# Performance work log

Measured on AMD Instinct MI355X. Metric: run time of the kernel, lower is better.

## Reference

```python
import jax, jax.numpy as jnp
from jax import lax
import numpy as np

EPS = 1e-5  # BatchNorm eps


def setup_inputs() -> dict:
    key = jax.random.key(0)
    ks = jax.random.split(key, 8)
    N, C_in, T, V = 64, 64, 300, 25
    C_out, K, KT = 64, 3, 9
    x = jax.random.normal(ks[0], (N, C_in, T, V), dtype=jnp.float32)
    A = jax.random.uniform(ks[1], (K, V, V), dtype=jnp.float32)
    # 1x1 conv weight squeezed to [K*C_out, C_in]
    w_gcn = jax.random.normal(ks[2], (K * C_out, C_in), dtype=jnp.float32) * (1.0 / np.sqrt(C_in))
    b_gcn = jax.random.normal(ks[3], (K * C_out,), dtype=jnp.float32) * 0.01
    # temporal conv weight [O, I, kT, 1]
    w_tcn = jax.random.normal(ks[4], (C_out, C_out, KT, 1), dtype=jnp.float32) * (1.0 / np.sqrt(C_out * KT))
    b_tcn = jax.random.normal(ks[5], (C_out,), dtype=jnp.float32) * 0.01
    gamma = jnp.ones((C_out,), dtype=jnp.float32)
    beta = jnp.zeros((C_out,), dtype=jnp.float32)
    return {"x": x, "A": A, "w_gcn": w_gcn, "b_gcn": b_gcn,
            "w_tcn": w_tcn, "b_tcn": b_tcn, "gamma": gamma, "beta": beta}


def reference(x, A, w_gcn, b_gcn, w_tcn, b_tcn, gamma, beta):
    K = A.shape[0]
    # unit_gcn: 1x1 conv (pointwise over channels) then spatial graph aggregation
    y = jnp.einsum('nctv,oc->notv', x, w_gcn) + b_gcn[None, :, None, None]  # [N, K*C, T, V]
    n, kc, t, v = y.shape
    y = y.reshape(n, K, kc // K, t, v)
    y = jnp.einsum('nkctv,kvw->nctw', y, A)  # [N, C, T, V]
    # unit_tcn: temporal conv (kernel 9x1, pad 4) + BatchNorm (training mode: batch stats)
    pad = (w_tcn.shape[2] - 1) // 2
    y = lax.conv_general_dilated(y, w_tcn, window_strides=(1, 1),
                                 padding=((pad, pad), (0, 0)),
                                 dimension_numbers=('NCHW', 'OIHW', 'NCHW'))
    y = y + b_tcn[None, :, None, None]
    mean = jnp.mean(y, axis=(0, 2, 3), keepdims=True)
    var = jnp.var(y, axis=(0, 2, 3), keepdims=True)
    y = (y - mean) * lax.rsqrt(var + EPS) * gamma[None, :, None, None] + beta[None, :, None, None]
    # residual (identity: in==out, stride==1) + ReLU
    return jax.nn.relu(y + x)
```

## Files before the change

### kernel.cpp

```cpp
#include <hip/hip_runtime.h>
#include <hip/hip_bf16.h>

#define N_    64
#define C_    64
#define T_    300
#define V_    25
#define K_    3
#define KT_   9
#define PAD_  4

typedef short bf16x8 __attribute__((ext_vector_type(8)));
typedef float f32x4  __attribute__((ext_vector_type(4)));

static __device__ __forceinline__ unsigned short f2bf(float f) {
    __hip_bfloat16 h = __float2bfloat16(f);
    return __builtin_bit_cast(unsigned short, h);
}
static __device__ __forceinline__ unsigned int pk2(float a, float b) {
    return (unsigned int)f2bf(a) | ((unsigned int)f2bf(b) << 16);
}
static __device__ __forceinline__ float bfhi(unsigned int u) {
    return __builtin_bit_cast(float, u << 16);
}
static __device__ __forceinline__ float bflo(unsigned int u) {
    return __builtin_bit_cast(float, u & 0xffff0000u);
}
static __device__ __forceinline__ float bf2f(unsigned short u) {
    return __builtin_bit_cast(float, (unsigned int)u << 16);
}

__global__ __launch_bounds__(256) void prep_kernel(
    const float* __restrict__ Wt, const float* __restrict__ Wg,
    const float* __restrict__ bg, const float* __restrict__ A,
    unsigned short* __restrict__ Wtb, unsigned short* __restrict__ Wgbt,
    unsigned short* __restrict__ bias2b, unsigned short* __restrict__ Abt)
{
    int i = blockIdx.x * 256 + threadIdx.x;
    if (i < 9*64*64) {
        int kt = i >> 12, r = i & 4095, o = r >> 6, c = r & 63;
        Wtb[i] = f2bf(Wt[(size_t)(o*64 + c)*9 + kt]);
    }
    int j = i - 9*64*64;
    if (j >= 0 && j < 64*192) {
        int o = j / 192, kc = j - 192*(j/192);
        int k = kc >> 6, ci = kc & 63;
        Wgbt[j] = f2bf(Wg[(size_t)(k*64 + o)*64 + ci]);
    }
    int m = j - 64*192;
    if (m >= 0 && m < 64*25) {
        int c = m / 25, w = m - 25*(m/25);
        float s = 0.f;
        for (int k = 0; k < 3; ++k) {
            float col = 0.f;
            for (int v = 0; v < 25; ++v) col += A[k*625 + v*25 + w];
            s += bg[k*64 + c] * col;
        }
        bias2b[w*64 + c] = f2bf(s);
    }
    int p = m - 64*25;
    if (p >= 0 && p < 3*32*40) {
        int k = p / 1280, r = p - 1280*k, w = r / 40, v = r - 40*(r/40);
        float val = (w < 25 && v < 25) ? A[k*625 + v*25 + w] : 0.f;
        Abt[p] = f2bf(val);
    }
}

#define GSUB   15
#define GGRP   (T_/GSUB)
#define NGBLK  (N_*GGRP)

__global__ __launch_bounds__(256, 5) void gcn_kernel(
    const float* __restrict__ x,
    const unsigned short* __restrict__ Wgbt,
    const unsigned short* __restrict__ Abt,
    const unsigned short* __restrict__ bias2b,
    unsigned short* __restrict__ y2)
{
    __shared__ unsigned short xslab[64*40];
    __shared__ unsigned short xa[32*200];
    __shared__ unsigned int   bias2L[25*34];

    const int tid  = threadIdx.x;
    const int n    = blockIdx.x / GGRP;
    const int tg   = (blockIdx.x % GGRP) * GSUB;
    const int lane = tid & 63, wave = tid >> 6;
    const int l15  = lane & 15, lq = lane >> 4;

    bf16x8 wfrag[6], afrag[6];
    #pragma unroll
    for (int cb = 0; cb < 6; ++cb) {
        wfrag[cb] = *(const bf16x8*)(Wgbt + (wave*16 + l15)*192 + cb*32 + lq*8);
        asm volatile("" : "+v"(wfrag[cb]));
    }
    #pragma unroll
    for (int s = 0; s < 6; ++s) {
        afrag[s] = *(const bf16x8*)(Abt + ((s >> 1)*32 + (s & 1)*16 + l15)*40 + lq*8);
        asm volatile("" : "+v"(afrag[s]));
    }

    for (int i = tid; i < 800; i += 256)
        bias2L[(i >> 5)*34 + (i & 31)] = ((const unsigned int*)bias2b)[i];
    if (tid < 192) {
        int r = tid / 3, z = tid - 3*(tid/3);
        ((unsigned int*)xslab)[r*20 + 13 + z] = 0u;
    }
    #pragma unroll
    for (int s = 0; s < 4; ++s) {
        int slot = tid + s*256;
        if (slot < 64*13) {
            int row = slot/13, sl = slot - 13*row;
            const float* xr = x + ((size_t)(n*C_ + row)*T_ + tg)*V_;
            float f0, f1;
            if (sl < 12) { float2 t2 = *(const float2*)(xr + 2*sl); f0 = t2.x; f1 = t2.y; }
            else         { f0 = xr[24]; f1 = 0.f; }
            ((unsigned int*)xslab)[row*20 + sl] = pk2(f0, f1);
        }
    }
    __syncthreads();

    for (int j = 0; j < GSUB; ++j) {
        const int t = tg + j;
        float2 Lr[4];
        const bool hn = (j + 1 < GSUB);
        if (hn) {
            #pragma unroll
            for (int s = 0; s < 4; ++s) {
                int slot = tid + s*256;
                if (slot < 64*13) {
                    int row = slot/13, sl = slot - 13*row;
                    const float* xr = x + ((size_t)(n*C_ + row)*T_ + t + 1)*V_;
                    if (sl < 12) Lr[s] = *(const float2*)(xr + 2*sl);
                    else         { Lr[s].x = xr[24]; Lr[s].y = 0.f; }
                }
            }
        }
        {
            bf16x8 xf = *(const bf16x8*)(xslab + (wave*16 + l15)*40 + lq*8);
            #pragma unroll
            for (int s = 0; s < 6; ++s) {
                f32x4 d = {};
                d = __builtin_amdgcn_mfma_f32_16x16x32_bf16(xf, afrag[s], d, 0, 0, 0);
                const int w = (s & 1)*16 + l15;
                if (w < 25) {
                    const int k = s >> 1;
                    unsigned long long pv = (unsigned long long)pk2(d[0], d[1])
                                          | ((unsigned long long)pk2(d[2], d[3]) << 32);
                    *(unsigned long long*)((char*)xa + w*400 + k*128 + wave*32 + lq*8) = pv;
                }
            }
        }
        __syncthreads();
        {
            f32x4 acc0 = {}, acc1 = {};
            #pragma unroll
            for (int cb = 0; cb < 6; ++cb) {
                bf16x8 b0 = *(const bf16x8*)((const char*)xa + l15*400      + cb*64 + lq*16);
                bf16x8 b1 = *(const bf16x8*)((const char*)xa + (16+l15)*400 + cb*64 + lq*16);
                acc0 = __builtin_amdgcn_mfma_f32_16x16x32_bf16(wfrag[cb], b0, acc0, 0, 0, 0);
                acc1 = __builtin_amdgcn_mfma_f32_16x16x32_bf16(wfrag[cb], b1, acc1, 0, 0, 0);
            }
            const int o0 = wave*16 + lq*4;
            {
                const int col = l15;
                unsigned int bu0 = bias2L[col*34 + (o0 >> 1)];
                unsigned int bu1 = bias2L[col*34 + (o0 >> 1) + 1];
                float v0 = acc0[0] + bfhi(bu0), v1 = acc0[1] + bflo(bu0);
                float v2 = acc0[2] + bfhi(bu1), v3 = acc0[3] + bflo(bu1);
                const size_t gcol = ((size_t)n*T_ + t)*V_ + col;
                *(unsigned long long*)(y2 + gcol*64 + o0) =
                      (unsigned long long)pk2(v0, v1)
                    | ((unsigned long long)pk2(v2, v3) << 32);
            }
            if (l15 < 9) {
                const int col = 16 + l15;
                unsigned int bu0 = bias2L[col*34 + (o0 >> 1)];
                unsigned int bu1 = bias2L[col*34 + (o0 >> 1) + 1];
                float v0 = acc1[0] + bfhi(bu0), v1 = acc1[1] + bflo(bu0);
                float v2 = acc1[2] + bfhi(bu1), v3 = acc1[3] + bflo(bu1);
                const size_t gcol = ((size_t)n*T_ + t)*V_ + col;
                *(unsigned long long*)(y2 + gcol*64 + o0) =
                      (unsigned long long)pk2(v0, v1)
                    | ((unsigned long long)pk2(v2, v3) << 32);
            }
        }
        if (hn) {
            #pragma unroll
            for (int s = 0; s < 4; ++s) {
                int slot = tid + s*256;
                if (slot < 64*13) {
                    int row = slot/13, sl = slot - 13*row;
                    ((unsigned int*)xslab)[row*20 + sl] = pk2(Lr[s].x, Lr[s].y);
                }
            }
        }
        __syncthreads();
    }
}

#define TTT    20
#define TCOLS  (TTT*V_)
#define SLABC  712
#define TTILES (T_/TTT)
#define NBLK   (N_*TTILES)

template<int BF>
__global__ __launch_bounds__(512, 2) void tcn_kernel(
    const unsigned short* __restrict__ y2, const unsigned short* __restrict__ Wtb,
    const float* __restrict__ bt,
    unsigned short* __restrict__ y3b, float* __restrict__ y3f,
    float* __restrict__ psum, float* __restrict__ psq)
{
    __shared__ unsigned short slab[SLABC*40];
    __shared__ float s_sum[64], s_sq[64];

    const int tid = threadIdx.x;
    const int n  = blockIdx.x / TTILES;
    const int t0 = (blockIdx.x % TTILES) * TTT;
    const int lane = tid & 63, wave = tid >> 6;
    const int l15 = lane & 15, lq = lane >> 4;
    const int colw = wave * 64;

    if (tid < 64) { s_sum[tid] = 0.f; s_sq[tid] = 0.f; }

    const int lo = (t0 < PAD_) ? (PAD_ - t0)*V_ : 0;
    const int hi = (t0 + TTT + PAD_ > T_) ? (T_ + PAD_ - t0)*V_ : SLABC;
    const long gbase = ((long)n*T_*V_ + (long)(t0 - PAD_)*V_)*64;

    f32x4 acc[4][4] = {};

    #pragma unroll
    for (int h = 0; h < 2; ++h) {
        __syncthreads();
        for (int i = tid; i < SLABC*4; i += 512) {
            int col = i >> 2, ck = i & 3;
            float4 val = {0.f, 0.f, 0.f, 0.f};
            if (col >= lo && col < hi)
                val = *(const float4*)(y2 + gbase + (long)col*64 + h*32 + ck*8);
            *(float4*)((char*)slab + col*80 + ck*16) = val;
        }
        __syncthreads();
        #pragma unroll
        for (int kt = 0; kt < 9; ++kt) {
            bf16x8 a[4];
            #pragma unroll
            for (int mt = 0; mt < 4; ++mt)
                a[mt] = *(const bf16x8*)(Wtb + kt*4096 + (mt*16 + l15)*64
                                         + h*32 + lq*8);
            #pragma unroll
            for (int nf = 0; nf < 4; ++nf) {
                const int col = colw + nf*16 + l15 + kt*25;
                bf16x8 b = *(const bf16x8*)((const char*)slab + col*80 + lq*16);
                #pragma unroll
                for (int mt = 0; mt < 4; ++mt)
                    acc[mt][nf] = __builtin_amdgcn_mfma_f32_16x16x32_bf16(
                        a[mt], b, acc[mt][nf], 0, 0, 0);
            }
        }
    }

    float ls[16], lsq[16];
    #pragma unroll
    for (int e = 0; e < 16; ++e) { ls[e] = 0.f; lsq[e] = 0.f; }

    #pragma unroll
    for (int mt = 0; mt < 4; ++mt) {
        #pragma unroll
        for (int r = 0; r < 4; ++r) {
            const int e = mt*4 + r;
            const int o = mt*16 + lq*4 + r;
            const float bias = bt[o];
            #pragma unroll
            for (int nf = 0; nf < 4; ++nf) {
                const int col = colw + nf*16 + l15;
                if (col < TCOLS) {
                    const float val = acc[mt][nf][r] + bias;
                    const size_t idx = (size_t)(n*C_ + o)*(T_*V_) + t0*V_ + col;
                    if (BF) y3b[idx] = f2bf(val);
                    else    y3f[idx] = val;
                    ls[e] += val; lsq[e] += val*val;
                }
            }
        }
    }

    __syncthreads();
    #pragma unroll
    for (int e = 0; e < 16; ++e) {
        float a = ls[e], b = lsq[e];
        a += __shfl_xor(a, 1); a += __shfl_xor(a, 2);
        a += __shfl_xor(a, 4); a += __shfl_xor(a, 8);
        b += __shfl_xor(b, 1); b += __shfl_xor(b, 2);
        b += __shfl_xor(b, 4); b += __shfl_xor(b, 8);
        if (l15 == 0) {
            const int o = (e >> 2)*16 + lq*4 + (e & 3);
            atomicAdd(&s_sum[o], a);
            atomicAdd(&s_sq[o], b);
        }
    }
    __syncthreads();
    if (tid < 64) {
        psum[(size_t)tid*NBLK + blockIdx.x] = s_sum[tid];
        psq [(size_t)tid*NBLK + blockIdx.x] = s_sq [tid];
    }
}

__global__ __launch_bounds__(256) void stats_kernel(
    const float* __restrict__ psum, const float* __restrict__ psq,
    const float* __restrict__ gamma, const float* __restrict__ beta,
    float* __restrict__ sb)
{
    const int o = blockIdx.x;
    const int tid = threadIdx.x;
    float s = 0.f, q = 0.f;
    for (int i = tid; i < NBLK; i += 256) {
        s += psum[(size_t)o*NBLK + i];
        q += psq [(size_t)o*NBLK + i];
    }
    __shared__ float rs[256], rq[256];
    rs[tid] = s; rq[tid] = q;
    __syncthreads();
    for (int off = 128; off > 0; off >>= 1) {
        if (tid < off) { rs[tid] += rs[tid + off]; rq[tid] += rq[tid + off]; }
        __syncthreads();
    }
    if (tid == 0) {
        const float cnt = (float)(N_ * T_ * V_);
        float mean = rs[0] / cnt;
        float var  = rq[0] / cnt - mean * mean;
        float rstd = rsqrtf(var + 1e-5f);
        float sc   = gamma[o] * rstd;
        sb[o]      = sc;
        sb[C_ + o] = beta[o] - mean * sc;
    }
}

__global__ __launch_bounds__(256) void bn_res_relu_bf16_kernel(
    const float* __restrict__ x, const unsigned short* __restrict__ y3b,
    const float* __restrict__ sb, float* __restrict__ out)
{
    const size_t total4 = (size_t)N_ * C_ * T_ * V_ / 4;
    size_t i4 = (size_t)blockIdx.x * 256 + threadIdx.x;
    if (i4 >= total4) return;
    const int c = (int)((i4 / (T_ * V_ / 4)) % C_);
    const float sc = sb[c], sh = sb[C_ + c];
    ushort4 yv = ((const ushort4*)y3b)[i4];
    float4 xv = ((const float4*)x)[i4];
    float4 o;
    o.x = fmaxf(bf2f(yv.x) * sc + sh + xv.x, 0.0f);
    o.y = fmaxf(bf2f(yv.y) * sc + sh + xv.y, 0.0f);
    o.z = fmaxf(bf2f(yv.z) * sc + sh + xv.z, 0.0f);
    o.w = fmaxf(bf2f(yv.w) * sc + sh + xv.w, 0.0f);
    ((float4*)out)[i4] = o;
}

__global__ __launch_bounds__(256) void bn_res_relu_f32_kernel(
    const float* __restrict__ x, const float* __restrict__ sb,
    float* __restrict__ y)
{
    const size_t total4 = (size_t)N_ * C_ * T_ * V_ / 4;
    size_t i4 = (size_t)blockIdx.x * 256 + threadIdx.x;
    if (i4 >= total4) return;
    const int c = (int)((i4 / (T_ * V_ / 4)) % C_);
    const float sc = sb[c], sh = sb[C_ + c];
    float4 yv = ((const float4*)y)[i4];
    float4 xv = ((const float4*)x)[i4];
    float4 o;
    o.x = fmaxf(yv.x * sc + sh + xv.x, 0.0f);
    o.y = fmaxf(yv.y * sc + sh + xv.y, 0.0f);
    o.z = fmaxf(yv.z * sc + sh + xv.z, 0.0f);
    o.w = fmaxf(yv.w * sc + sh + xv.w, 0.0f);
    ((float4*)y)[i4] = o;
}

extern "C" void kernel_launch(void* const* d_in, const int* in_sizes, int n_in,
                              void* d_out, int out_size, void* d_ws, size_t ws_size,
                              hipStream_t stream)
{
    const float* x     = (const float*)d_in[0];
    const float* A     = (const float*)d_in[1];
    const float* wg    = (const float*)d_in[2];
    const float* bg    = (const float*)d_in[3];
    const float* wt    = (const float*)d_in[4];
    const float* bt    = (const float*)d_in[5];
    const float* gamma = (const float*)d_in[6];
    const float* beta  = (const float*)d_in[7];
    float* out = (float*)d_out;

    char* wsb = (char*)d_ws;
    const size_t Y2B   = 61440000;
    const size_t Y3B   = 61440000;
    const size_t PSB   = (size_t)C_ * NBLK * 4;
    const size_t TABLE = 2*PSB + 512 + 73728 + 24576 + 3200 + 7680;
    const bool usebf = ws_size >= Y2B + Y3B + TABLE;

    unsigned short* y2  = (unsigned short*)wsb;
    unsigned short* y3b = (unsigned short*)(wsb + Y2B);
    const size_t base2  = usebf ? (Y2B + Y3B) : Y2B;
    float* psum            = (float*)(wsb + base2);
    float* psq             = (float*)(wsb + base2 + PSB);
    float* sb              = (float*)(wsb + base2 + 2*PSB);
    unsigned short* Wtb    = (unsigned short*)(wsb + base2 + 2*PSB + 512);
    unsigned short* Wgbt   = (unsigned short*)(wsb + base2 + 2*PSB + 512 + 73728);
    unsigned short* bias2b = (unsigned short*)(wsb + base2 + 2*PSB + 512 + 73728 + 24576);
    unsigned short* Abt    = (unsigned short*)(wsb + base2 + 2*PSB + 512 + 73728 + 24576 + 3200);

    prep_kernel<<<214, 256, 0, stream>>>(wt, wg, bg, A, Wtb, Wgbt, bias2b, Abt);
    gcn_kernel<<<NGBLK, 256, 0, stream>>>(x, Wgbt, Abt, bias2b, y2);
    if (usebf)
        tcn_kernel<1><<<NBLK, 512, 0, stream>>>(y2, Wtb, bt, y3b, out, psum, psq);
    else
        tcn_kernel<0><<<NBLK, 512, 0, stream>>>(y2, Wtb, bt, y3b, out, psum, psq);
    stats_kernel<<<C_, 256, 0, stream>>>(psum, psq, gamma, beta, sb);
    const size_t total4 = (size_t)N_ * C_ * T_ * V_ / 4;
    const int bnblk = (int)((total4 + 255) / 256);
    if (usebf)
        bn_res_relu_bf16_kernel<<<bnblk, 256, 0, stream>>>(x, y3b, sb, out);
    else
        bn_res_relu_f32_kernel<<<bnblk, 256, 0, stream>>>(x, sb, out);
}
```

Measured before the change: 290.6 us.

## Prefetch second TCN channel half during MFMA, grid-stride BN kernel, larger GCN tile

The TCN kernel now loads the second 32-channel half of the input slab into registers while the MFMA loop runs on the first half, hiding global-load latency behind compute. The BN/residual/ReLU kernels become grid-stride loops launched with a fixed 2048 blocks instead of one thread per float4. The GCN time sub-tile grows from 15 to 20 steps, which cuts the block count. The costs are extra registers in the TCN kernel (6 float4 staging values), which may hurt occupancy under launch bounds of 512 threads and 2 blocks, and fewer GCN blocks, which changes load balance.

Measured after the change: 307.6 us. +5.9%, slower.

```diff
diff --git a/kernel.cpp b/kernel.cpp
--- a/kernel.cpp
+++ b/kernel.cpp
@@ -65,7 +65,7 @@
     }
 }
 
-#define GSUB   15
+#define GSUB   20
 #define GGRP   (T_/GSUB)
 #define NGBLK  (N_*GGRP)
 
@@ -202,6 +202,7 @@
 #define SLABC  712
 #define TTILES (T_/TTT)
 #define NBLK   (N_*TTILES)
+#define NCHK   (SLABC*4)
 
 template<int BF>
 __global__ __launch_bounds__(512, 2) void tcn_kernel(
@@ -226,35 +227,84 @@
     const int hi = (t0 + TTT + PAD_ > T_) ? (T_ + PAD_ - t0)*V_ : SLABC;
     const long gbase = ((long)n*T_*V_ + (long)(t0 - PAD_)*V_)*64;
 
+    float4 st[6];
+
+    #pragma unroll
+    for (int k = 0; k < 6; ++k) {
+        int i = tid + k*512;
+        float4 v = {0.f, 0.f, 0.f, 0.f};
+        if (i < NCHK) {
+            int col = i >> 2, ck = i & 3;
+            if (col >= lo && col < hi)
+                v = *(const float4*)(y2 + gbase + (long)col*64 + ck*8);
+        }
+        st[k] = v;
+    }
+    #pragma unroll
+    for (int k = 0; k < 6; ++k) {
+        int i = tid + k*512;
+        if (i < NCHK) {
+            int col = i >> 2, ck = i & 3;
+            *(float4*)((char*)slab + col*80 + ck*16) = st[k];
+        }
+    }
+    __syncthreads();
+
+    #pragma unroll
+    for (int k = 0; k < 6; ++k) {
+        int i = tid + k*512;
+        float4 v = {0.f, 0.f, 0.f, 0.f};
+        if (i < NCHK) {
+            int col = i >> 2, ck = i & 3;
+            if (col >= lo && col < hi)
+                v = *(const float4*)(y2 + gbase + (long)col*64 + 32 + ck*8);
+        }
+        st[k] = v;
+    }
+
     f32x4 acc[4][4] = {};
-
-    #pragma unroll
-    for (int h = 0; h < 2; ++h) {
-        __syncthreads();
-        for (int i = tid; i < SLABC*4; i += 512) {
+    #pragma unroll
+    for (int kt = 0; kt < 9; ++kt) {
+        bf16x8 a[4];
+        #pragma unroll
+        for (int mt = 0; mt < 4; ++mt)
+            a[mt] = *(const bf16x8*)(Wtb + kt*4096 + (mt*16 + l15)*64 + lq*8);
+        #pragma unroll
+        for (int nf = 0; nf < 4; ++nf) {
+            const int col = colw + nf*16 + l15 + kt*25;
+            bf16x8 b = *(const bf16x8*)((const char*)slab + col*80 + lq*16);
+            #pragma unroll
+            for (int mt = 0; mt < 4; ++mt)
+                acc[mt][nf] = __builtin_amdgcn_mfma_f32_16x16x32_bf16(
+                    a[mt], b, acc[mt][nf], 0, 0, 0);
+        }
+    }
+    __syncthreads();
+
+    #pragma unroll
+    for (int k = 0; k < 6; ++k) {
+        int i = tid + k*512;
+        if (i < NCHK) {
             int col = i >> 2, ck = i & 3;
-            float4 val = {0.f, 0.f, 0.f, 0.f};
-            if (col >= lo && col < hi)
-                val = *(const float4*)(y2 + gbase + (long)col*64 + h*32 + ck*8);
-            *(float4*)((char*)slab + col*80 + ck*16) = val;
-        }
-        __syncthreads();
+            *(float4*)((char*)slab + col*80 + ck*16) = st[k];
+        }
+    }
+    __syncthreads();
+
+    #pragma unroll
+    for (int kt = 0; kt < 9; ++kt) {
+        bf16x8 a[4];
         #pragma unroll
-        for (int kt = 0; kt < 9; ++kt) {
-            bf16x8 a[4];
+        for (int mt = 0; mt < 4; ++mt)
+            a[mt] = *(const bf16x8*)(Wtb + kt*4096 + (mt*16 + l15)*64 + 32 + lq*8);
+        #pragma unroll
+        for (int nf = 0; nf < 4; ++nf) {
+            const int col = colw + nf*16 + l15 + kt*25;
+            bf16x8 b = *(const bf16x8*)((const char*)slab + col*80 + lq*16);
             #pragma unroll
             for (int mt = 0; mt < 4; ++mt)
-                a[mt] = *(const bf16x8*)(Wtb + kt*4096 + (mt*16 + l15)*64
-                                         + h*32 + lq*8);
-            #pragma unroll
-            for (int nf = 0; nf < 4; ++nf) {
-                const int col = colw + nf*16 + l15 + kt*25;
-                bf16x8 b = *(const bf16x8*)((const char*)slab + col*80 + lq*16);
-                #pragma unroll
-                for (int mt = 0; mt < 4; ++mt)
-                    acc[mt][nf] = __builtin_amdgcn_mfma_f32_16x16x32_bf16(
-                        a[mt], b, acc[mt][nf], 0, 0, 0);
-            }
+                acc[mt][nf] = __builtin_amdgcn_mfma_f32_16x16x32_bf16(
+                    a[mt], b, acc[mt][nf], 0, 0, 0);
         }
     }
 
@@ -339,18 +389,19 @@
     const float* __restrict__ sb, float* __restrict__ out)
 {
     const size_t total4 = (size_t)N_ * C_ * T_ * V_ / 4;
-    size_t i4 = (size_t)blockIdx.x * 256 + threadIdx.x;
-    if (i4 >= total4) return;
-    const int c = (int)((i4 / (T_ * V_ / 4)) % C_);
-    const float sc = sb[c], sh = sb[C_ + c];
-    ushort4 yv = ((const ushort4*)y3b)[i4];
-    float4 xv = ((const float4*)x)[i4];
-    float4 o;
-    o.x = fmaxf(bf2f(yv.x) * sc + sh + xv.x, 0.0f);
-    o.y = fmaxf(bf2f(yv.y) * sc + sh + xv.y, 0.0f);
-    o.z = fmaxf(bf2f(yv.z) * sc + sh + xv.z, 0.0f);
-    o.w = fmaxf(bf2f(yv.w) * sc + sh + xv.w, 0.0f);
-    ((float4*)out)[i4] = o;
+    const size_t stride = (size_t)gridDim.x * 256;
+    for (size_t i4 = (size_t)blockIdx.x * 256 + threadIdx.x; i4 < total4; i4 += stride) {
+        const int c = (int)((i4 / (T_ * V_ / 4)) % C_);
+        const float sc = sb[c], sh = sb[C_ + c];
+        ushort4 yv = ((const ushort4*)y3b)[i4];
+        float4 xv = ((const float4*)x)[i4];
+        float4 o;
+        o.x = fmaxf(bf2f(yv.x) * sc + sh + xv.x, 0.0f);
+        o.y = fmaxf(bf2f(yv.y) * sc + sh + xv.y, 0.0f);
+        o.z = fmaxf(bf2f(yv.z) * sc + sh + xv.z, 0.0f);
+        o.w = fmaxf(bf2f(yv.w) * sc + sh + xv.w, 0.0f);
+        ((float4*)out)[i4] = o;
+    }
 }
 
 __global__ __launch_bounds__(256) void bn_res_relu_f32_kernel(
@@ -358,18 +409,19 @@
     float* __restrict__ y)
 {
     const size_t total4 = (size_t)N_ * C_ * T_ * V_ / 4;
-    size_t i4 = (size_t)blockIdx.x * 256 + threadIdx.x;
-    if (i4 >= total4) return;
-    const int c = (int)((i4 / (T_ * V_ / 4)) % C_);
-    const float sc = sb[c], sh = sb[C_ + c];
-    float4 yv = ((const float4*)y)[i4];
-    float4 xv = ((const float4*)x)[i4];
-    float4 o;
-    o.x = fmaxf(yv.x * sc + sh + xv.x, 0.0f);
-    o.y = fmaxf(yv.y * sc + sh + xv.y, 0.0f);
-    o.z = fmaxf(yv.z * sc + sh + xv.z, 0.0f);
-    o.w = fmaxf(yv.w * sc + sh + xv.w, 0.0f);
-    ((float4*)y)[i4] = o;
+    const size_t stride = (size_t)gridDim.x * 256;
+    for (size_t i4 = (size_t)blockIdx.x * 256 + threadIdx.x; i4 < total4; i4 += stride) {
+        const int c = (int)((i4 / (T_ * V_ / 4)) % C_);
+        const float sc = sb[c], sh = sb[C_ + c];
+        float4 yv = ((const float4*)y)[i4];
+        float4 xv = ((const float4*)x)[i4];
+        float4 o;
+        o.x = fmaxf(yv.x * sc + sh + xv.x, 0.0f);
+        o.y = fmaxf(yv.y * sc + sh + xv.y, 0.0f);
+        o.z = fmaxf(yv.z * sc + sh + xv.z, 0.0f);
+        o.w = fmaxf(yv.w * sc + sh + xv.w, 0.0f);
+        ((float4*)y)[i4] = o;
+    }
 }
 
 extern "C" void kernel_launch(void* const* d_in, const int* in_sizes, int n_in,
@@ -411,10 +463,8 @@
     else
         tcn_kernel<0><<<NBLK, 512, 0, stream>>>(y2, Wtb, bt, y3b, out, psum, psq);
     stats_kernel<<<C_, 256, 0, stream>>>(psum, psq, gamma, beta, sb);
-    const size_t total4 = (size_t)N_ * C_ * T_ * V_ / 4;
-    const int bnblk = (int)((total4 + 255) / 256);
     if (usebf)
-        bn_res_relu_bf16_kernel<<<bnblk, 256, 0, stream>>>(x, y3b, sb, out);
+        bn_res_relu_bf16_kernel<<<2048, 256, 0, stream>>>(x, y3b, sb, out);
     else
-        bn_res_relu_f32_kernel<<<bnblk, 256, 0, stream>>>(x, sb, out);
-}
+        bn_res_relu_f32_kernel<<<2048, 256, 0, stream>>>(x, sb, out);
+}
```
